# Optimization experiments

Hardware: AMD Instinct MI355X
Metric: run time of the kernel (lower is better)

Reference implementation:

```python
import jax, jax.numpy as jnp
import numpy as np

B, N, HID, E, H = 4, 256, 256, 64, 4
OUT = HID // 2          # 128
D = OUT // H            # 32
AGG = H * (2 * D + 1)   # 260 = concat(mean D, attn_sum 1, max D) per head


def setup_inputs() -> dict:
    key = jax.random.key(0)
    ks = jax.random.split(key, 7)
    s = 0.05
    return {
        "h_x": jax.random.normal(ks[0], (B, N, HID), jnp.float32),
        "h_e": jax.random.normal(ks[1], (B, N, N, E), jnp.float32),
        "h_m": jnp.ones((B, N), jnp.float32),
        "W_Q": jax.random.normal(ks[2], (OUT, HID), jnp.float32) * s,
        "W_K": jax.random.normal(ks[3], (OUT, E), jnp.float32) * s,
        "W_V": jax.random.normal(ks[4], (OUT, E), jnp.float32) * s,
        "W_R": jax.random.normal(ks[5], (OUT, AGG), jnp.float32) * s,
    }


def reference(h_x, h_e, h_m, W_Q, W_K, W_V, W_R):
    # queries from node features: [B,H,N,D]
    h_q = (h_x @ W_Q.T).reshape(B, N, H, D).transpose(0, 2, 1, 3)
    # keys/values from dense pairwise edge features: [B,H,N,N,D]
    h_k = jnp.einsum('bnme,ce->bnmc', h_e, W_K).reshape(B, N, N, H, D).transpose(0, 3, 1, 2, 4)
    h_v = jnp.einsum('bnme,ce->bnmc', h_e, W_V).reshape(B, N, N, H, D).transpose(0, 3, 1, 2, 4)
    # broadcast dot: [B,H,N,N]
    scores = jnp.einsum('bhnd,bhnmd->bhnm', h_q, h_k) / np.float32(np.sqrt(D))
    # per-node mask broadcast as [B,1,N,1] (masks query rows)
    scores = jnp.where(h_m[:, None, :, None] == 0, -jnp.inf, scores)
    # NOTE: original code softmaxes over dim=1 = HEAD axis (faithful)
    attn = jax.nn.softmax(scores, axis=1)                      # [B,H,N,N]
    attn_w = attn[..., None] * h_v                             # [B,H,N,N,D]
    aggr_sum = attn_w.sum(axis=3)                              # [B,H,N,D]
    attn_sum = attn.sum(axis=3, keepdims=True) + 1e-8          # [B,H,N,1]
    aggr_mean = aggr_sum / attn_sum
    aggr_max = attn_w.max(axis=3)                              # [B,H,N,D]
    multi = jnp.concatenate([aggr_mean, attn_sum, aggr_max], axis=-1)  # [B,H,N,2D+1]
    aggr_out = multi.transpose(0, 2, 1, 3).reshape(B, N, AGG)  # [B,N,260]
    return aggr_out @ W_R.T                                    # [B,N,OUT]
```

## Files before the change

kernel.cpp:

```cpp
#include <hip/hip_runtime.h>
#include <hip/hip_bf16.h>

constexpr int Bb   = 4;
constexpr int Nn   = 256;
constexpr int HID  = 256;
constexpr int Ee   = 64;
constexpr int Hh   = 4;
constexpr int OUTc = 128;
constexpr int Dd   = 32;
constexpr int AGG  = 260;
constexpr int REC  = 264;
constexpr int QA_LD = 264;

constexpr size_t WS_WRT   = 0;
constexpr size_t WS_FRAGV = WS_WRT + (size_t)AGG * OUTc;
constexpr size_t WS_FRAGQ = WS_FRAGV + 4096;
constexpr size_t WS_UFRAG = WS_FRAGQ + 16384;

typedef __attribute__((ext_vector_type(8))) short short8;
typedef __attribute__((ext_vector_type(4))) float floatx4;

__device__ __forceinline__ unsigned pk2(float a, float b) {
    union { __hip_bfloat162 h; unsigned u; } cv;
    cv.h = __float22bfloat162_rn(float2{a, b});
    return cv.u;
}

__device__ __forceinline__ short8 pack8(floatx4 f0, floatx4 f1) {
    union { short8 s; unsigned u[4]; } r;
    r.u[0] = pk2(f0[0], f0[1]);
    r.u[1] = pk2(f0[2], f0[3]);
    r.u[2] = pk2(f1[0], f1[1]);
    r.u[3] = pk2(f1[2], f1[3]);
    return r.s;
}

__global__ __launch_bounds__(256)
void eama_pack(const float* __restrict__ W_Q, const float* __restrict__ W_V,
               const float* __restrict__ W_R,
               unsigned short* __restrict__ wfragV, unsigned short* __restrict__ wfragQ,
               float* __restrict__ W_RT)
{
    const int tid = threadIdx.x;
    const int bid = blockIdx.x;

    if (bid < 4) {
        const int e    = bid * 256 + tid;
        const int lane = e & 63;
        const int ks   = (e >> 6) & 1;
        const int ct   = e >> 7;
        const int ncol = lane & 15, q8 = lane >> 4;
        const float* row = W_V + (ct * 16 + ncol) * Ee;
        const int k0 = ks * 32 + q8 * 8;
        floatx4 f0 = *(const floatx4*)(row + k0);
        floatx4 f1 = *(const floatx4*)(row + k0 + 4);
        *(short8*)(wfragV + (size_t)e * 8) = pack8(f0, f1);
    } else if (bid < 20) {
        const int e    = (bid - 4) * 256 + tid;
        const int lane = e & 63;
        const int ks   = (e >> 6) & 7;
        const int ct   = (e >> 9) & 1;
        const int wv   = (e >> 10) & 3;
        const int ncol = lane & 15, q8 = lane >> 4;
        const float* row = W_Q + (wv * 32 + ct * 16 + ncol) * HID;
        const int k0 = ks * 32 + q8 * 8;
        floatx4 f0 = *(const floatx4*)(row + k0);
        floatx4 f1 = *(const floatx4*)(row + k0 + 4);
        *(short8*)(wfragQ + (size_t)e * 8) = pack8(f0, f1);
    } else {
        const int i = (bid - 20) * 256 + tid;
        if (i < AGG * OUTc) {
            const int c = i & 127, j = i >> 7;
            W_RT[j * OUTc + c] = W_R[c * AGG + j];
        }
    }
}

__global__ __launch_bounds__(256)
void eama_qu(const float* __restrict__ h_x, const unsigned short* __restrict__ wfragQ,
             const float* __restrict__ W_K, unsigned short* __restrict__ ufrag)
{
    __shared__ __align__(16) unsigned short sA[16 * QA_LD];
    __shared__ __align__(16) float sqL[16][132];
    __shared__ __align__(16) float sU2[16][256];
    const int tid  = threadIdx.x;
    const int b0   = blockIdx.x * 16;
    const int lane = tid & 63;
    const int wv   = tid >> 6;
    const int ncol = lane & 15, q8 = lane >> 4;

    short8 bq[2][8];
    #pragma unroll
    for (int ct = 0; ct < 2; ++ct)
        #pragma unroll
        for (int ks = 0; ks < 8; ++ks) {
            const int e = ((wv * 2 + ct) * 8 + ks) * 64 + lane;
            bq[ct][ks] = *(const short8*)(wfragQ + (size_t)e * 8);
        }
    #pragma unroll
    for (int i = 0; i < 2; ++i) {
        const int idx = tid + i * 256;
        const int r = idx >> 5, blk = idx & 31;
        const float* src = h_x + (size_t)(b0 + r) * HID + blk * 8;
        floatx4 f0 = *(const floatx4*)(src);
        floatx4 f1 = *(const floatx4*)(src + 4);
        *(short8*)&sA[r * QA_LD + blk * 8] = pack8(f0, f1);
    }
    __syncthreads();
    floatx4 acc[2] = {(floatx4){0,0,0,0}, (floatx4){0,0,0,0}};
    #pragma unroll
    for (int ks = 0; ks < 8; ++ks) {
        short8 a = *(const short8*)&sA[ncol * QA_LD + ks * 32 + q8 * 8];
        acc[0] = __builtin_amdgcn_mfma_f32_16x16x32_bf16(a, bq[0][ks], acc[0], 0, 0, 0);
        acc[1] = __builtin_amdgcn_mfma_f32_16x16x32_bf16(a, bq[1][ks], acc[1], 0, 0, 0);
    }
    #pragma unroll
    for (int ct = 0; ct < 2; ++ct)
        #pragma unroll
        for (int rr = 0; rr < 4; ++rr)
            sqL[q8 * 4 + rr][wv * 32 + ct * 16 + ncol] = acc[ct][rr];
    __syncthreads();

    {
        const int h = wv, e = lane;
        float a16[16];
        #pragma unroll
        for (int i = 0; i < 16; ++i) a16[i] = 0.f;
        #pragma unroll
        for (int d4 = 0; d4 < 8; ++d4) {
            float wk0 = W_K[(h * Dd + d4 * 4 + 0) * Ee + e];
            float wk1 = W_K[(h * Dd + d4 * 4 + 1) * Ee + e];
            float wk2 = W_K[(h * Dd + d4 * 4 + 2) * Ee + e];
            float wk3 = W_K[(h * Dd + d4 * 4 + 3) * Ee + e];
            #pragma unroll
            for (int b16 = 0; b16 < 16; ++b16) {
                floatx4 qv = *(const floatx4*)&sqL[b16][h * Dd + d4 * 4];
                a16[b16] += (qv[0] * wk0 + qv[1] * wk1) + (qv[2] * wk2 + qv[3] * wk3);
            }
        }
        #pragma unroll
        for (int b16 = 0; b16 < 16; ++b16)
            sU2[b16][h * 64 + e] = a16[b16] * 0.1767766952966369f;
    }
    __syncthreads();

    #pragma unroll
    for (int k = 0; k < 8; ++k) {
        const int ei   = tid + k * 256;
        const int b16  = ei >> 7;
        const int rest = ei & 127;
        const int ks   = rest >> 6;
        const int l    = rest & 63;
        const int nc   = l & 15, qq = l >> 4;
        short8 v = {0, 0, 0, 0, 0, 0, 0, 0};
        if (nc < Hh) {
            floatx4 f0 = *(const floatx4*)&sU2[b16][nc * 64 + ks * 32 + qq * 8];
            floatx4 f1 = *(const floatx4*)&sU2[b16][nc * 64 + ks * 32 + qq * 8 + 4];
            v = pack8(f0, f1);
        }
        *(short8*)(ufrag + ((size_t)((b0 + b16) * 2 + ks) * 64 + l) * 8) = v;
    }
}

__global__ __launch_bounds__(256, 2)
void eama_full(const float* __restrict__ h_e, const float* __restrict__ h_m,
               const unsigned short* __restrict__ wfragV,
               const unsigned short* __restrict__ ufrag,
               const float* __restrict__ W_RT, float* __restrict__ out)
{
    __shared__ __align__(16) float sS[4][16][4];
    __shared__ float sVS[4][OUTc];
    __shared__ float sVM[4][OUTc];
    __shared__ float sAS[4][Hh];
    __shared__ float sAsum[Hh];
    __shared__ __align__(16) float sM[REC];
    __shared__ float sAcc[2][OUTc];

    const int tid  = threadIdx.x;
    const int lane = tid & 63;
    const int w    = tid >> 6;
    const int ncol = lane & 15;
    const int q8   = lane >> 4;
    const int bn   = blockIdx.x;
    const float maskv = h_m[bn];

    short8 bfV[8][2];
    #pragma unroll
    for (int ct = 0; ct < 8; ++ct)
        #pragma unroll
        for (int ks = 0; ks < 2; ++ks)
            bfV[ct][ks] = *(const short8*)(wfragV + ((size_t)(ct * 2 + ks) * 64 + lane) * 8);
    short8 bu0 = *(const short8*)(ufrag + ((size_t)(bn * 2 + 0) * 64 + lane) * 8);
    short8 bu1 = *(const short8*)(ufrag + ((size_t)(bn * 2 + 1) * 64 + lane) * 8);

    float vs[8], vm[8], asumH = 0.f;
    #pragma unroll
    for (int ct = 0; ct < 8; ++ct) { vs[ct] = 0.f; vm[ct] = -3.402823466e38f; }

    const float* heb = h_e + (size_t)bn * Nn * Ee;

    floatx4 p0, p1, p2, p3;
    {
        const float* ar = heb + (size_t)(w * 64 + ncol) * Ee;
        p0 = *(const floatx4*)(ar + q8 * 8);
        p1 = *(const floatx4*)(ar + q8 * 8 + 4);
        p2 = *(const floatx4*)(ar + 32 + q8 * 8);
        p3 = *(const floatx4*)(ar + 32 + q8 * 8 + 4);
    }

    #pragma unroll
    for (int it = 0; it < 4; ++it) {
        floatx4 n0, n1, n2, n3;
        if (it < 3) {
            const float* ar = heb + (size_t)(w * 64 + (it + 1) * 16 + ncol) * Ee;
            n0 = *(const floatx4*)(ar + q8 * 8);
            n1 = *(const floatx4*)(ar + q8 * 8 + 4);
            n2 = *(const floatx4*)(ar + 32 + q8 * 8);
            n3 = *(const floatx4*)(ar + 32 + q8 * 8 + 4);
        }
        short8 af0 = pack8(p0, p1);
        short8 af1 = pack8(p2, p3);

        floatx4 accV[8], accS = (floatx4){0, 0, 0, 0};
        #pragma unroll
        for (int ct = 0; ct < 8; ++ct) accV[ct] = (floatx4){0, 0, 0, 0};
        #pragma unroll
        for (int ct = 0; ct < 8; ++ct) {
            accV[ct] = __builtin_amdgcn_mfma_f32_16x16x32_bf16(af0, bfV[ct][0], accV[ct], 0, 0, 0);
            accV[ct] = __builtin_amdgcn_mfma_f32_16x16x32_bf16(af1, bfV[ct][1], accV[ct], 0, 0, 0);
        }
        accS = __builtin_amdgcn_mfma_f32_16x16x32_bf16(af0, bu0, accS, 0, 0, 0);
        accS = __builtin_amdgcn_mfma_f32_16x16x32_bf16(af1, bu1, accS, 0, 0, 0);

        if (ncol < Hh) {
            #pragma unroll
            for (int r = 0; r < 4; ++r)
                sS[w][q8 * 4 + r][ncol] = (maskv != 0.f) ? accS[r] : -1e30f;
        }
        __builtin_amdgcn_wave_barrier();

        #pragma unroll
        for (int r = 0; r < 4; ++r) {
            floatx4 sc = *(const floatx4*)&sS[w][q8 * 4 + r][0];
            float e0 = __expf(sc[0]), e1 = __expf(sc[1]);
            float e2 = __expf(sc[2]), e3 = __expf(sc[3]);
            float inv = 1.f / ((e0 + e1) + (e2 + e3));
            float a0 = e0 * inv, a1 = e1 * inv, a2 = e2 * inv, a3 = e3 * inv;
            asumH += (ncol & 2) ? ((ncol & 1) ? a3 : a2) : ((ncol & 1) ? a1 : a0);
            float p;
            p = a0 * accV[0][r]; vs[0] += p; vm[0] = fmaxf(vm[0], p);
            p = a0 * accV[1][r]; vs[1] += p; vm[1] = fmaxf(vm[1], p);
            p = a1 * accV[2][r]; vs[2] += p; vm[2] = fmaxf(vm[2], p);
            p = a1 * accV[3][r]; vs[3] += p; vm[3] = fmaxf(vm[3], p);
            p = a2 * accV[4][r]; vs[4] += p; vm[4] = fmaxf(vm[4], p);
            p = a2 * accV[5][r]; vs[5] += p; vm[5] = fmaxf(vm[5], p);
            p = a3 * accV[6][r]; vs[6] += p; vm[6] = fmaxf(vm[6], p);
            p = a3 * accV[7][r]; vs[7] += p; vm[7] = fmaxf(vm[7], p);
        }
        __builtin_amdgcn_wave_barrier();
        p0 = n0; p1 = n1; p2 = n2; p3 = n3;
    }

    #pragma unroll
    for (int ct = 0; ct < 8; ++ct) {
        vs[ct] += __shfl_xor(vs[ct], 16, 64);
        vs[ct] += __shfl_xor(vs[ct], 32, 64);
        vm[ct] = fmaxf(vm[ct], __shfl_xor(vm[ct], 16, 64));
        vm[ct] = fmaxf(vm[ct], __shfl_xor(vm[ct], 32, 64));
    }
    asumH += __shfl_xor(asumH, 16, 64);
    asumH += __shfl_xor(asumH, 32, 64);

    if (lane < 16) {
        #pragma unroll
        for (int ct = 0; ct < 8; ++ct) {
            sVS[w][ct * 16 + lane] = vs[ct];
            sVM[w][ct * 16 + lane] = vm[ct];
        }
    }
    if (lane < Hh) sAS[w][lane] = asumH;
    __syncthreads();
    if (tid < Hh) {
        sAsum[tid] = 1e-8f +
            (sAS[0][tid] + sAS[1][tid]) + (sAS[2][tid] + sAS[3][tid]);
    }
    __syncthreads();
    if (tid < OUTc) {
        float vsum = (sVS[0][tid] + sVS[1][tid]) + (sVS[2][tid] + sVS[3][tid]);
        float vmax = fmaxf(fmaxf(sVM[0][tid], sVM[1][tid]), fmaxf(sVM[2][tid], sVM[3][tid]));
        const int h = tid >> 5, d = tid & 31;
        sM[h * 65 + d]      = vsum / sAsum[h];
        sM[h * 65 + 33 + d] = vmax;
        if (tid < Hh) sM[tid * 65 + 32] = sAsum[tid];
    }
    __syncthreads();
    {
        const int c = tid & 127, part = tid >> 7;
        const int j0 = part * 130;
        float a0 = 0.f, a1 = 0.f, a2 = 0.f, a3 = 0.f;
        #pragma unroll 4
        for (int j = j0; j < j0 + 128; j += 4) {
            a0 = fmaf(sM[j],     W_RT[(j)     * OUTc + c], a0);
            a1 = fmaf(sM[j + 1], W_RT[(j + 1) * OUTc + c], a1);
            a2 = fmaf(sM[j + 2], W_RT[(j + 2) * OUTc + c], a2);
            a3 = fmaf(sM[j + 3], W_RT[(j + 3) * OUTc + c], a3);
        }
        a0 = fmaf(sM[j0 + 128], W_RT[(j0 + 128) * OUTc + c], a0);
        a1 = fmaf(sM[j0 + 129], W_RT[(j0 + 129) * OUTc + c], a1);
        sAcc[part][c] = (a0 + a1) + (a2 + a3);
    }
    __syncthreads();
    if (tid < OUTc)
        out[bn * OUTc + tid] = sAcc[0][tid] + sAcc[1][tid];
}

extern "C" void kernel_launch(void* const* d_in, const int* in_sizes, int n_in,
                              void* d_out, int out_size, void* d_ws, size_t ws_size,
                              hipStream_t stream) {
    const float* h_x = (const float*)d_in[0];
    const float* h_e = (const float*)d_in[1];
    const float* h_m = (const float*)d_in[2];
    const float* W_Q = (const float*)d_in[3];
    const float* W_K = (const float*)d_in[4];
    const float* W_V = (const float*)d_in[5];
    const float* W_R = (const float*)d_in[6];
    float* out = (float*)d_out;

    float* ws            = (float*)d_ws;
    float* W_RT          = ws + WS_WRT;
    unsigned short* wfV  = (unsigned short*)(ws + WS_FRAGV);
    unsigned short* wfQ  = (unsigned short*)(ws + WS_FRAGQ);
    unsigned short* ufr  = (unsigned short*)(ws + WS_UFRAG);

    eama_pack<<<dim3(150), dim3(256), 0, stream>>>(W_Q, W_V, W_R, wfV, wfQ, W_RT);
    eama_qu<<<dim3(Bb * Nn / 16), dim3(256), 0, stream>>>(h_x, wfQ, W_K, ufr);
    eama_full<<<dim3(Bb * Nn), dim3(256), 0, stream>>>(h_e, h_m, wfV, ufr, W_RT, out);
}
```

Before: 127.1 us.

## Merge prep kernels and stage edge loads through LDS with async double buffering

The weight-pack and query-projection kernels are merged into one launch, and W_Q is packed inline instead of through a workspace fragment buffer. This removes one kernel launch and a dependency hop. The main kernel now streams h_e through per-wave LDS double buffers using global_load_lds, with explicit vmcnt waits, instead of register prefetch. The launch bound is raised to 4 blocks per SM for more occupancy, and sM/sAcc are aliased onto the staging buffer to limit LDS use. The hand-written waitcnt sequencing is fragile, and the tighter register budget could cause spills.

Measured after the change: 173.0 us. 36.1% more time.

```diff
diff --git a/kernel.cpp b/kernel.cpp
--- a/kernel.cpp
+++ b/kernel.cpp
@@ -35,12 +35,23 @@
     return r.s;
 }
 
+__device__ __forceinline__ void gload16(const float* g, float* l) {
+    __builtin_amdgcn_global_load_lds(
+        (const __attribute__((address_space(1))) void*)g,
+        (__attribute__((address_space(3))) void*)l, 16, 0, 0);
+}
+
 __global__ __launch_bounds__(256)
-void eama_pack(const float* __restrict__ W_Q, const float* __restrict__ W_V,
-               const float* __restrict__ W_R,
-               unsigned short* __restrict__ wfragV, unsigned short* __restrict__ wfragQ,
-               float* __restrict__ W_RT)
+void eama_prep(const float* __restrict__ W_Q, const float* __restrict__ W_V,
+               const float* __restrict__ W_R, const float* __restrict__ h_x,
+               const float* __restrict__ W_K,
+               unsigned short* __restrict__ wfragV, float* __restrict__ W_RT,
+               unsigned short* __restrict__ ufrag)
 {
+    __shared__ __align__(16) unsigned short sA[16 * QA_LD];
+    __shared__ __align__(16) float sqL[16][132];
+    __shared__ __align__(16) float sU2[16][256];
+
     const int tid = threadIdx.x;
     const int bid = blockIdx.x;
 
@@ -55,36 +66,18 @@
         floatx4 f0 = *(const floatx4*)(row + k0);
         floatx4 f1 = *(const floatx4*)(row + k0 + 4);
         *(short8*)(wfragV + (size_t)e * 8) = pack8(f0, f1);
-    } else if (bid < 20) {
-        const int e    = (bid - 4) * 256 + tid;
-        const int lane = e & 63;
-        const int ks   = (e >> 6) & 7;
-        const int ct   = (e >> 9) & 1;
-        const int wv   = (e >> 10) & 3;
-        const int ncol = lane & 15, q8 = lane >> 4;
-        const float* row = W_Q + (wv * 32 + ct * 16 + ncol) * HID;
-        const int k0 = ks * 32 + q8 * 8;
-        floatx4 f0 = *(const floatx4*)(row + k0);
-        floatx4 f1 = *(const floatx4*)(row + k0 + 4);
-        *(short8*)(wfragQ + (size_t)e * 8) = pack8(f0, f1);
-    } else {
-        const int i = (bid - 20) * 256 + tid;
+        return;
+    }
+    if (bid < 134) {
+        const int i = (bid - 4) * 256 + tid;
         if (i < AGG * OUTc) {
             const int c = i & 127, j = i >> 7;
             W_RT[j * OUTc + c] = W_R[c * AGG + j];
         }
-    }
-}
-
-__global__ __launch_bounds__(256)
-void eama_qu(const float* __restrict__ h_x, const unsigned short* __restrict__ wfragQ,
-             const float* __restrict__ W_K, unsigned short* __restrict__ ufrag)
-{
-    __shared__ __align__(16) unsigned short sA[16 * QA_LD];
-    __shared__ __align__(16) float sqL[16][132];
-    __shared__ __align__(16) float sU2[16][256];
-    const int tid  = threadIdx.x;
-    const int b0   = blockIdx.x * 16;
+        return;
+    }
+
+    const int b0   = (bid - 134) * 16;
     const int lane = tid & 63;
     const int wv   = tid >> 6;
     const int ncol = lane & 15, q8 = lane >> 4;
@@ -94,8 +87,8 @@
     for (int ct = 0; ct < 2; ++ct)
         #pragma unroll
         for (int ks = 0; ks < 8; ++ks) {
-            const int e = ((wv * 2 + ct) * 8 + ks) * 64 + lane;
-            bq[ct][ks] = *(const short8*)(wfragQ + (size_t)e * 8);
+            const float* row = W_Q + (size_t)(wv * 32 + ct * 16 + ncol) * HID + ks * 32 + q8 * 8;
+            bq[ct][ks] = pack8(*(const floatx4*)row, *(const floatx4*)(row + 4));
         }
     #pragma unroll
     for (int i = 0; i < 2; ++i) {
@@ -162,19 +155,21 @@
     }
 }
 
-__global__ __launch_bounds__(256, 2)
+__global__ __launch_bounds__(256, 4)
 void eama_full(const float* __restrict__ h_e, const float* __restrict__ h_m,
                const unsigned short* __restrict__ wfragV,
                const unsigned short* __restrict__ ufrag,
                const float* __restrict__ W_RT, float* __restrict__ out)
 {
+    __shared__ __align__(16) float sStage[4][2][4][64][4];
     __shared__ __align__(16) float sS[4][16][4];
     __shared__ float sVS[4][OUTc];
     __shared__ float sVM[4][OUTc];
     __shared__ float sAS[4][Hh];
     __shared__ float sAsum[Hh];
-    __shared__ __align__(16) float sM[REC];
-    __shared__ float sAcc[2][OUTc];
+
+    float* sM = &sStage[0][0][0][0][0];
+    float (*sAcc)[OUTc] = (float (*)[OUTc])(sM + 384);
 
     const int tid  = threadIdx.x;
     const int lane = tid & 63;
@@ -192,34 +187,42 @@
             bfV[ct][ks] = *(const short8*)(wfragV + ((size_t)(ct * 2 + ks) * 64 + lane) * 8);
     short8 bu0 = *(const short8*)(ufrag + ((size_t)(bn * 2 + 0) * 64 + lane) * 8);
     short8 bu1 = *(const short8*)(ufrag + ((size_t)(bn * 2 + 1) * 64 + lane) * 8);
+    asm volatile("" ::: "memory");
+
+    const float* heb = h_e + (size_t)bn * Nn * Ee;
+    const float* arq = heb + (size_t)(w * 64 + ncol) * Ee + q8 * 8;
+
+    #define STAGE(it_, buf_) do { \
+        const float* ar_ = arq + (size_t)(it_) * 16 * Ee; \
+        gload16(ar_,      &sStage[w][buf_][0][0][0]); \
+        gload16(ar_ + 4,  &sStage[w][buf_][1][0][0]); \
+        gload16(ar_ + 32, &sStage[w][buf_][2][0][0]); \
+        gload16(ar_ + 36, &sStage[w][buf_][3][0][0]); \
+    } while (0)
+
+    STAGE(0, 0);
+    STAGE(1, 1);
 
     float vs[8], vm[8], asumH = 0.f;
     #pragma unroll
     for (int ct = 0; ct < 8; ++ct) { vs[ct] = 0.f; vm[ct] = -3.402823466e38f; }
 
-    const float* heb = h_e + (size_t)bn * Nn * Ee;
-
-    floatx4 p0, p1, p2, p3;
-    {
-        const float* ar = heb + (size_t)(w * 64 + ncol) * Ee;
-        p0 = *(const floatx4*)(ar + q8 * 8);
-        p1 = *(const floatx4*)(ar + q8 * 8 + 4);
-        p2 = *(const floatx4*)(ar + 32 + q8 * 8);
-        p3 = *(const floatx4*)(ar + 32 + q8 * 8 + 4);
-    }
-
     #pragma unroll
     for (int it = 0; it < 4; ++it) {
-        floatx4 n0, n1, n2, n3;
-        if (it < 3) {
-            const float* ar = heb + (size_t)(w * 64 + (it + 1) * 16 + ncol) * Ee;
-            n0 = *(const floatx4*)(ar + q8 * 8);
-            n1 = *(const floatx4*)(ar + q8 * 8 + 4);
-            n2 = *(const floatx4*)(ar + 32 + q8 * 8);
-            n3 = *(const floatx4*)(ar + 32 + q8 * 8 + 4);
-        }
-        short8 af0 = pack8(p0, p1);
-        short8 af1 = pack8(p2, p3);
+        const int buf = it & 1;
+        if (it < 3) asm volatile("s_waitcnt vmcnt(4)" ::: "memory");
+        else        asm volatile("s_waitcnt vmcnt(0)" ::: "memory");
+
+        floatx4 c0 = *(const floatx4*)&sStage[w][buf][0][lane][0];
+        floatx4 c1 = *(const floatx4*)&sStage[w][buf][1][lane][0];
+        floatx4 c2 = *(const floatx4*)&sStage[w][buf][2][lane][0];
+        floatx4 c3 = *(const floatx4*)&sStage[w][buf][3][lane][0];
+        short8 af0 = pack8(c0, c1);
+        short8 af1 = pack8(c2, c3);
+        if (it < 2) {
+            asm volatile("s_waitcnt lgkmcnt(0)" ::: "memory");
+            STAGE(it + 2, buf);
+        }
 
         floatx4 accV[8], accS = (floatx4){0, 0, 0, 0};
         #pragma unroll
@@ -258,8 +261,8 @@
             p = a3 * accV[7][r]; vs[7] += p; vm[7] = fmaxf(vm[7], p);
         }
         __builtin_amdgcn_wave_barrier();
-        p0 = n0; p1 = n1; p2 = n2; p3 = n3;
-    }
+    }
+    #undef STAGE
 
     #pragma unroll
     for (int ct = 0; ct < 8; ++ct) {
@@ -329,10 +332,8 @@
     float* ws            = (float*)d_ws;
     float* W_RT          = ws + WS_WRT;
     unsigned short* wfV  = (unsigned short*)(ws + WS_FRAGV);
-    unsigned short* wfQ  = (unsigned short*)(ws + WS_FRAGQ);
     unsigned short* ufr  = (unsigned short*)(ws + WS_UFRAG);
 
-    eama_pack<<<dim3(150), dim3(256), 0, stream>>>(W_Q, W_V, W_R, wfV, wfQ, W_RT);
-    eama_qu<<<dim3(Bb * Nn / 16), dim3(256), 0, stream>>>(h_x, wfQ, W_K, ufr);
+    eama_prep<<<dim3(198), dim3(256), 0, stream>>>(W_Q, W_V, W_R, h_x, W_K, wfV, W_RT, ufr);
     eama_full<<<dim3(Bb * Nn), dim3(256), 0, stream>>>(h_e, h_m, wfV, ufr, W_RT, out);
 }
```
